# Performance work log

Hardware: AMD Instinct MI355X
Metric: run time of the kernel (lower is better)

Reference implementation:

```python
import jax, jax.numpy as jnp
import numpy as np

B, L, H = 2, 2048, 1536
I, N, R, K = 3072, 16, 96, 4


def setup_inputs() -> dict:
    key = jax.random.key(0)
    ks = jax.random.split(key, 10)
    rn = lambda k, shape, s: jax.random.normal(k, shape, jnp.float32) * s
    return {
        "hidden_states": rn(ks[0], (B, L, H), 1.0),
        "W_in": rn(ks[1], (2 * I, H), 0.02),
        "conv_w": rn(ks[2], (I, K), 0.1),
        "conv_b": rn(ks[3], (I,), 0.1),
        "W_x": rn(ks[4], (R + 2 * N, I), 0.02),
        "W_dt": rn(ks[5], (I, R), 0.02),
        "dt_bias": rn(ks[6], (I,), 0.1),
        # vLLM's weight loader stores A = -exp(A_log); replicate that here
        "A": -jnp.exp(rn(ks[7], (I, N), 0.5)),
        "D": jnp.ones((I,), jnp.float32),
        "W_out": rn(ks[8], (H, I), 0.02),
    }


def reference(hidden_states, W_in, conv_w, conv_b, W_x, W_dt, dt_bias, A, D, W_out):
    b, l, _ = hidden_states.shape
    k = conv_w.shape[1]
    n = A.shape[1]
    r = W_dt.shape[1]

    # in_proj -> [B,L,2I], split into ssm input x and gate
    proj = jnp.einsum("blh,eh->ble", hidden_states, W_in)
    x, gate = jnp.split(proj, 2, axis=-1)  # each [B,L,I]

    # causal depthwise conv1d over L (pad K-1 on the left) + SiLU
    xp = jnp.pad(x, ((0, 0), (k - 1, 0), (0, 0)))
    conv = sum(xp[:, j : j + l, :] * conv_w[:, j] for j in range(k)) + conv_b
    x = jax.nn.silu(conv)  # [B,L,I]

    # x_proj -> dt (rank R), B, C (each N)
    ssm_p = jnp.einsum("bli,pi->blp", x, W_x)
    dt_in, Bm, Cm = jnp.split(ssm_p, [r, r + n], axis=-1)

    # dt_proj (skip_bias_add) then softplus(dt + bias) inside the scan math
    dt = jnp.einsum("blr,ir->bli", dt_in, W_dt)
    delta = jax.nn.softplus(dt + dt_bias)  # [B,L,I]

    # selective scan: s_t = exp(delta_t * A) * s_{t-1} + delta_t * x_t * B_t
    def step(state, inp):
        d_t, u_t, B_t, C_t = inp  # [B,I], [B,I], [B,N], [B,N]
        dA = jnp.exp(d_t[..., None] * A)  # [B,I,N]
        state = state * dA + (d_t * u_t)[..., None] * B_t[:, None, :]
        y = jnp.einsum("bin,bn->bi", state, C_t)
        return state, y

    init = jnp.zeros((b, x.shape[-1], n), jnp.float32)
    _, ys = jax.lax.scan(
        step,
        init,
        (
            delta.transpose(1, 0, 2),
            x.transpose(1, 0, 2),
            Bm.transpose(1, 0, 2),
            Cm.transpose(1, 0, 2),
        ),
    )
    y = ys.transpose(1, 0, 2) + x * D  # skip connection via D
    y = y * jax.nn.silu(gate)

    # out_proj -> [B,L,H]
    return jnp.einsum("bli,hi->blh", y, W_out)
```

## Files before the change

kernel.cpp:

```cpp
#include <hip/hip_runtime.h>

typedef __attribute__((ext_vector_type(8))) short bf16x8;
typedef __attribute__((ext_vector_type(4))) float f32x4;

#define CCH 32
#define TCH 64

__device__ __forceinline__ unsigned short f2b(float f) {
    unsigned u = __float_as_uint(f);
    return (unsigned short)((u + 0x7fffu + ((u >> 16) & 1u)) >> 16);
}
__device__ __forceinline__ float b2f(unsigned short h) {
    return __uint_as_float(((unsigned)h) << 16);
}
__device__ __forceinline__ float softplus_f(float z) {
    return (z > 15.f) ? z : __logf(1.f + __expf(z));
}
__device__ __forceinline__ float silu_f(float g) {
    return g / (1.f + __expf(-g));
}

__device__ __forceinline__ void gload16(const unsigned short* g, unsigned short* l) {
    __builtin_amdgcn_global_load_lds(
        (const __attribute__((address_space(1))) void*)g,
        (__attribute__((address_space(3))) void*)l, 16, 0, 0);
}

__global__ __launch_bounds__(256)
void cast4(const float* __restrict__ s, unsigned short* __restrict__ d, int n4) {
    int i = blockIdx.x * 256 + threadIdx.x;
    if (i >= n4) return;
    float4 v = reinterpret_cast<const float4*>(s)[i];
    ushort4 o;
    o.x = f2b(v.x); o.y = f2b(v.y); o.z = f2b(v.z); o.w = f2b(v.w);
    reinterpret_cast<ushort4*>(d)[i] = o;
}

template <int OP>
__global__ __launch_bounds__(256)
void gemm_mfma(const unsigned short* __restrict__ A, const unsigned short* __restrict__ W,
               void* __restrict__ Cout, int Kc, int lda, int ldw, int ldc,
               const float* __restrict__ bias, int silu_col0, long long czs) {
    __shared__ unsigned short As[128 * 32];
    __shared__ unsigned short Bs[128 * 32];
    const int tid = threadIdx.x;
    const int bm = blockIdx.y * 128;
    const int bn = blockIdx.x * 128;
    const int kz = blockIdx.z;
    A += (size_t)kz * Kc;
    W += (size_t)kz * Kc;
    const int lane = tid & 63;
    const int wave = tid >> 6;
    const int r_a = lane >> 2;
    const int k8 = (lane & 3) * 8;

    unsigned short* ldsA0 = As + (size_t)(wave)     * 512;
    unsigned short* ldsA1 = As + (size_t)(wave + 4) * 512;
    unsigned short* ldsB0 = Bs + (size_t)(wave)     * 512;
    unsigned short* ldsB1 = Bs + (size_t)(wave + 4) * 512;
    const unsigned short* gA0 = A + (size_t)(bm + wave * 16 + r_a) * lda + k8;
    const unsigned short* gA1 = A + (size_t)(bm + 64 + wave * 16 + r_a) * lda + k8;
    const unsigned short* gB0 = W + (size_t)(bn + wave * 16 + r_a) * ldw + k8;
    const unsigned short* gB1 = W + (size_t)(bn + 64 + wave * 16 + r_a) * ldw + k8;

    const int wm = (wave & 1) * 64;
    const int wn = (wave >> 1) * 64;
    const int lr = lane & 15;
    const int quad = lane >> 4;

    f32x4 acc[4][4];
    const f32x4 zero = {0.f, 0.f, 0.f, 0.f};
#pragma unroll
    for (int i = 0; i < 4; i++)
#pragma unroll
        for (int j = 0; j < 4; j++) acc[i][j] = zero;

    for (int k0 = 0; k0 < Kc; k0 += 32) {
        __syncthreads();
        gload16(gA0 + k0, ldsA0);
        gload16(gA1 + k0, ldsA1);
        gload16(gB0 + k0, ldsB0);
        gload16(gB1 + k0, ldsB1);
        __syncthreads();
        bf16x8 fa[4], fb[4];
#pragma unroll
        for (int mi = 0; mi < 4; mi++)
            fa[mi] = *reinterpret_cast<const bf16x8*>(As + (wm + mi * 16 + lr) * 32 + quad * 8);
#pragma unroll
        for (int ni = 0; ni < 4; ni++)
            fb[ni] = *reinterpret_cast<const bf16x8*>(Bs + (wn + ni * 16 + lr) * 32 + quad * 8);
#pragma unroll
        for (int mi = 0; mi < 4; mi++)
#pragma unroll
            for (int ni = 0; ni < 4; ni++)
                acc[mi][ni] = __builtin_amdgcn_mfma_f32_16x16x32_bf16(fa[mi], fb[ni], acc[mi][ni], 0, 0, 0);
    }

#pragma unroll
    for (int mi = 0; mi < 4; mi++)
#pragma unroll
        for (int reg = 0; reg < 4; reg++) {
            int row = bm + wm + mi * 16 + quad * 4 + reg;
#pragma unroll
            for (int ni = 0; ni < 4; ni++) {
                int col = bn + wn + ni * 16 + lr;
                float v = acc[mi][ni][reg];
                if (OP == 0) {
                    float* Cf = (float*)Cout + (size_t)kz * czs;
                    Cf[(size_t)row * ldc + col] = v;
                } else if (OP == 2) {
                    if (col >= silu_col0) v = silu_f(v);
                    ((unsigned short*)Cout)[(size_t)row * ldc + col] = f2b(v);
                } else {
                    ((unsigned short*)Cout)[(size_t)row * ldc + col] = f2b(softplus_f(v + bias[col]));
                }
            }
        }
}

__global__ __launch_bounds__(256)
void reduce_xpart(const float* __restrict__ xpart, float* __restrict__ ssmp,
                  unsigned short* __restrict__ dtin) {
    const int BL = 4096;
    int idx = blockIdx.x * 256 + threadIdx.x;
    int row = idx >> 5;
    int c4 = (idx & 31) * 4;
    float4 s = {0.f, 0.f, 0.f, 0.f};
#pragma unroll
    for (int z = 0; z < 8; z++) {
        float4 v = *reinterpret_cast<const float4*>(xpart + (size_t)z * BL * 128 + (size_t)row * 128 + c4);
        s.x += v.x; s.y += v.y; s.z += v.z; s.w += v.w;
    }
    *reinterpret_cast<float4*>(ssmp + (size_t)row * 128 + c4) = s;
    if (c4 < 96) {
        ushort4 o;
        o.x = f2b(s.x); o.y = f2b(s.y); o.z = f2b(s.z); o.w = f2b(s.w);
        *reinterpret_cast<ushort4*>(dtin + (size_t)row * 96 + c4) = o;
    }
}

__global__ __launch_bounds__(256)
void conv_silu8(const unsigned short* __restrict__ projbf, const float* __restrict__ cw,
                const float* __restrict__ cb, unsigned short* __restrict__ xc) {
    const int I = 3072, L = 2048, LD = 6144;
    int idx = blockIdx.x * 256 + threadIdx.x;
    int i8 = (idx % (I / 8)) * 8;
    int bl = idx / (I / 8);
    int l = bl & (L - 1);
    float s[8];
    {
        float4 b0 = *reinterpret_cast<const float4*>(cb + i8);
        float4 b1 = *reinterpret_cast<const float4*>(cb + i8 + 4);
        s[0]=b0.x; s[1]=b0.y; s[2]=b0.z; s[3]=b0.w; s[4]=b1.x; s[5]=b1.y; s[6]=b1.z; s[7]=b1.w;
    }
    float w[8][4];
#pragma unroll
    for (int c = 0; c < 8; c++) {
        float4 wr = *reinterpret_cast<const float4*>(cw + (i8 + c) * 4);
        w[c][0]=wr.x; w[c][1]=wr.y; w[c][2]=wr.z; w[c][3]=wr.w;
    }
#pragma unroll
    for (int j = 0; j < 4; j++) {
        if (l + j - 3 >= 0) {
            uint4 r = *reinterpret_cast<const uint4*>(projbf + (size_t)(bl + j - 3) * LD + i8);
            float xv[8];
            xv[0]=b2f((unsigned short)(r.x & 0xffff)); xv[1]=b2f((unsigned short)(r.x >> 16));
            xv[2]=b2f((unsigned short)(r.y & 0xffff)); xv[3]=b2f((unsigned short)(r.y >> 16));
            xv[4]=b2f((unsigned short)(r.z & 0xffff)); xv[5]=b2f((unsigned short)(r.z >> 16));
            xv[6]=b2f((unsigned short)(r.w & 0xffff)); xv[7]=b2f((unsigned short)(r.w >> 16));
#pragma unroll
            for (int c = 0; c < 8; c++) s[c] = fmaf(xv[c], w[c][j], s[c]);
        }
    }
    unsigned short o[8];
#pragma unroll
    for (int c = 0; c < 8; c++) o[c] = f2b(silu_f(s[c]));
    uint4 packed;
    packed.x = (unsigned)o[0] | ((unsigned)o[1] << 16);
    packed.y = (unsigned)o[2] | ((unsigned)o[3] << 16);
    packed.z = (unsigned)o[4] | ((unsigned)o[5] << 16);
    packed.w = (unsigned)o[6] | ((unsigned)o[7] << 16);
    *reinterpret_cast<uint4*>(xc + (size_t)bl * I + i8) = packed;
}

__global__ __launch_bounds__(256)
void scan_passA(const unsigned short* __restrict__ delta_bf, const unsigned short* __restrict__ xc,
                const float* __restrict__ ssmp, const float* __restrict__ Aw,
                float* __restrict__ S_local, float* __restrict__ sumDelta) {
    const int I = 3072, L = 2048;
    __shared__ float bc[TCH][32];
    int g = blockIdx.x * 256 + threadIdx.x;
    int i = g % I;
    int bcid = g / I;
    int c = bcid % CCH;
    int b = bcid / CCH;
    size_t rowbase = (size_t)b * L + (size_t)c * TCH;
    for (int e = threadIdx.x; e < TCH * 8; e += 256) {
        int t = e >> 3, q = e & 7;
        float4 v = *reinterpret_cast<const float4*>(ssmp + (rowbase + t) * 128 + 96 + q * 4);
        *reinterpret_cast<float4*>(&bc[t][q * 4]) = v;
    }
    __syncthreads();

    float Arow[16];
#pragma unroll
    for (int n = 0; n < 16; n++) Arow[n] = Aw[i * 16 + n];
    float st[16];
#pragma unroll
    for (int n = 0; n < 16; n++) st[n] = 0.f;
    float sumD = 0.f;

    size_t rowI = rowbase * I + i;
    for (int t = 0; t < TCH; t++) {
        float delta = b2f(delta_bf[rowI]);
        float du = delta * b2f(xc[rowI]);
        sumD += delta;
        float4 b0 = *reinterpret_cast<const float4*>(&bc[t][0]);
        float4 b1 = *reinterpret_cast<const float4*>(&bc[t][4]);
        float4 b2 = *reinterpret_cast<const float4*>(&bc[t][8]);
        float4 b3 = *reinterpret_cast<const float4*>(&bc[t][12]);
        const float bv[16] = {b0.x,b0.y,b0.z,b0.w, b1.x,b1.y,b1.z,b1.w,
                              b2.x,b2.y,b2.z,b2.w, b3.x,b3.y,b3.z,b3.w};
#pragma unroll
        for (int n = 0; n < 16; n++)
            st[n] = fmaf(st[n], __expf(delta * Arow[n]), du * bv[n]);
        rowI += I;
    }
    size_t obase = (size_t)bcid * 16 * I + i;
#pragma unroll
    for (int n = 0; n < 16; n++) S_local[obase + (size_t)n * I] = st[n];
    sumDelta[(size_t)bcid * I + i] = sumD;
}

__global__ __launch_bounds__(256)
void scan_passB(const float* __restrict__ S_local, const float* __restrict__ sumDelta,
                const float* __restrict__ Aw, float* __restrict__ state_in) {
    const int I = 3072;
    int g = blockIdx.x * 256 + threadIdx.x;
    int i = g % I;
    int bn = g / I;
    int n = bn & 15;
    int b = bn >> 4;
    float a = Aw[i * 16 + n];
    float state = 0.f;
    for (int c = 0; c < CCH; c++) {
        int bcid = b * CCH + c;
        size_t idx = ((size_t)bcid * 16 + n) * I + i;
        state_in[idx] = state;
        state = fmaf(state, __expf(a * sumDelta[(size_t)bcid * I + i]), S_local[idx]);
    }
}

__global__ __launch_bounds__(256)
void scan_passC(const unsigned short* __restrict__ projbf,
                const unsigned short* __restrict__ xc,
                const float* __restrict__ ssmp, const unsigned short* __restrict__ delta_bf,
                const float* __restrict__ Aw, const float* __restrict__ Dw,
                const float* __restrict__ state_in, unsigned short* __restrict__ ybf) {
    const int I = 3072, L = 2048, LD = 6144;
    __shared__ float bc[TCH][32];
    int g = blockIdx.x * 256 + threadIdx.x;
    int i = g % I;
    int bcid = g / I;
    int c = bcid % CCH;
    int b = bcid / CCH;
    size_t rowbase = (size_t)b * L + (size_t)c * TCH;
    for (int e = threadIdx.x; e < TCH * 8; e += 256) {
        int t = e >> 3, q = e & 7;
        float4 v = *reinterpret_cast<const float4*>(ssmp + (rowbase + t) * 128 + 96 + q * 4);
        *reinterpret_cast<float4*>(&bc[t][q * 4]) = v;
    }
    __syncthreads();

    float Arow[16];
#pragma unroll
    for (int n = 0; n < 16; n++) Arow[n] = Aw[i * 16 + n];
    float Dv = Dw[i];
    float st[16];
    size_t sbase = (size_t)bcid * 16 * I + i;
#pragma unroll
    for (int n = 0; n < 16; n++) st[n] = state_in[sbase + (size_t)n * I];

    size_t rowI = rowbase * I + i;
    size_t rowG = rowbase * LD + I + i;
    for (int t = 0; t < TCH; t++) {
        float delta = b2f(delta_bf[rowI]);
        float u = b2f(xc[rowI]);
        float du = delta * u;
        float4 b0 = *reinterpret_cast<const float4*>(&bc[t][0]);
        float4 b1 = *reinterpret_cast<const float4*>(&bc[t][4]);
        float4 b2 = *reinterpret_cast<const float4*>(&bc[t][8]);
        float4 b3 = *reinterpret_cast<const float4*>(&bc[t][12]);
        float4 c0 = *reinterpret_cast<const float4*>(&bc[t][16]);
        float4 c1 = *reinterpret_cast<const float4*>(&bc[t][20]);
        float4 c2 = *reinterpret_cast<const float4*>(&bc[t][24]);
        float4 c3 = *reinterpret_cast<const float4*>(&bc[t][28]);
        const float bv[16] = {b0.x,b0.y,b0.z,b0.w, b1.x,b1.y,b1.z,b1.w,
                              b2.x,b2.y,b2.z,b2.w, b3.x,b3.y,b3.z,b3.w};
        const float cv[16] = {c0.x,c0.y,c0.z,c0.w, c1.x,c1.y,c1.z,c1.w,
                              c2.x,c2.y,c2.z,c2.w, c3.x,c3.y,c3.z,c3.w};
        float y = 0.f;
#pragma unroll
        for (int n = 0; n < 16; n++) {
            st[n] = fmaf(st[n], __expf(delta * Arow[n]), du * bv[n]);
            y = fmaf(st[n], cv[n], y);
        }
        y = fmaf(u, Dv, y);
        y *= b2f(projbf[rowG]);
        ybf[rowI] = f2b(y);
        rowI += I;
        rowG += LD;
    }
}

extern "C" void kernel_launch(void* const* d_in, const int* in_sizes, int n_in,
                              void* d_out, int out_size, void* d_ws, size_t ws_size,
                              hipStream_t stream) {
    const float* hidden  = (const float*)d_in[0];
    const float* W_in    = (const float*)d_in[1];
    const float* conv_w  = (const float*)d_in[2];
    const float* conv_b  = (const float*)d_in[3];
    const float* W_x     = (const float*)d_in[4];
    const float* W_dt    = (const float*)d_in[5];
    const float* dt_bias = (const float*)d_in[6];
    const float* Aw      = (const float*)d_in[7];
    const float* Dw      = (const float*)d_in[8];
    const float* W_out   = (const float*)d_in[9];
    float* out = (float*)d_out;

    constexpr int Bsz = 2, L = 2048, H = 1536, I = 3072, R = 96;
    constexpr int BL = Bsz * L;
    constexpr int TwoI = 2 * I;

    char* base = (char*)d_ws;
    unsigned short* proj_bf  = (unsigned short*)base; base += (size_t)BL * TwoI * 2;
    unsigned short* delta_bf = (unsigned short*)base; base += (size_t)BL * I * 2;
    unsigned short* xc_bf    = (unsigned short*)base; base += (size_t)BL * I * 2;
    unsigned short* y_bf     = (unsigned short*)base; base += (size_t)BL * I * 2;
    float* ssmp              = (float*)base;          base += (size_t)BL * 128 * 4;
    float* xpart             = (float*)base;          base += (size_t)8 * BL * 128 * 4;
    unsigned short* dtin_bf  = (unsigned short*)base; base += (size_t)BL * R * 2;
    unsigned short* wx_bf    = (unsigned short*)base; base += (size_t)128 * I * 2;
    unsigned short* wdt_bf   = (unsigned short*)base; base += (size_t)I * R * 2;
    unsigned short* wout_bf  = (unsigned short*)base; base += (size_t)H * I * 2;
    unsigned short* h_bf     = (unsigned short*)base; base += (size_t)BL * H * 2;
    unsigned short* win_bf   = (unsigned short*)base; base += (size_t)TwoI * H * 2;
    float* S_local  = (float*)h_bf;
    float* sumDelta = S_local + (size_t)Bsz * CCH * 16 * I;
    float* state_in = sumDelta + (size_t)Bsz * CCH * I;

    dim3 blk(256);

    cast4<<<(BL * H / 4 + 255) / 256, blk, 0, stream>>>(hidden, h_bf, BL * H / 4);
    cast4<<<(TwoI * H / 4 + 255) / 256, blk, 0, stream>>>(W_in, win_bf, TwoI * H / 4);
    cast4<<<(128 * I / 4 + 255) / 256, blk, 0, stream>>>(W_x, wx_bf, 128 * I / 4);
    cast4<<<(I * R / 4 + 255) / 256, blk, 0, stream>>>(W_dt, wdt_bf, I * R / 4);
    cast4<<<(H * I / 4 + 255) / 256, blk, 0, stream>>>(W_out, wout_bf, H * I / 4);

    gemm_mfma<2><<<dim3(TwoI / 128, BL / 128, 1), blk, 0, stream>>>(
        h_bf, win_bf, proj_bf, H, H, H, TwoI, nullptr, I, 0);

    conv_silu8<<<BL * I / 8 / 256, blk, 0, stream>>>(proj_bf, conv_w, conv_b, xc_bf);

    gemm_mfma<0><<<dim3(1, BL / 128, 8), blk, 0, stream>>>(
        xc_bf, wx_bf, xpart, I / 8, I, I, 128, nullptr, 0, (long long)BL * 128);
    reduce_xpart<<<BL * 32 / 256, blk, 0, stream>>>(xpart, ssmp, dtin_bf);

    gemm_mfma<3><<<dim3(I / 128, BL / 128, 1), blk, 0, stream>>>(
        dtin_bf, wdt_bf, delta_bf, R, R, R, I, dt_bias, 0, 0);

    scan_passA<<<Bsz * I * CCH / 256, blk, 0, stream>>>(
        delta_bf, xc_bf, ssmp, Aw, S_local, sumDelta);
    scan_passB<<<Bsz * 16 * I / 256, blk, 0, stream>>>(
        S_local, sumDelta, Aw, state_in);
    scan_passC<<<Bsz * I * CCH / 256, blk, 0, stream>>>(
        proj_bf, xc_bf, ssmp, delta_bf, Aw, Dw, state_in, y_bf);

    gemm_mfma<0><<<dim3(H / 128, BL / 128, 1), blk, 0, stream>>>(
        y_bf, wout_bf, out, I, I, I, H, nullptr, 0, 0);
}
```

Measured before the change: 521.1 us.

## Double-buffer GEMM LDS tiles, fuse casts, split-K out_proj with atomics

The GEMM main loop now double-buffers its LDS tiles, prefetching the next K-slice with global_load_lds while MFMAs run on the current one, which removes one barrier per iteration. The five separate fp32-to-bf16 cast launches are merged into a single kernel with hardcoded segment bounds. The output projection is split into two K halves that accumulate into a zeroed output with float atomicAdd, doubling the block count. In exchange, LDS use doubles per block, the output needs a memset, atomics add nondeterministic summation order, and the cast bounds only hold for these exact shapes.

```diff
diff --git a/kernel.cpp b/kernel.cpp
--- a/kernel.cpp
+++ b/kernel.cpp
@@ -27,13 +27,26 @@
 }
 
 __global__ __launch_bounds__(256)
-void cast4(const float* __restrict__ s, unsigned short* __restrict__ d, int n4) {
+void cast_all(const float* __restrict__ h, const float* __restrict__ win,
+              const float* __restrict__ wx, const float* __restrict__ wdt,
+              const float* __restrict__ wout,
+              unsigned short* __restrict__ dh, unsigned short* __restrict__ dwin,
+              unsigned short* __restrict__ dwx, unsigned short* __restrict__ dwdt,
+              unsigned short* __restrict__ dwout) {
+    const int n0 = 1572864, n1 = n0 + 2359296, n2 = n1 + 98304,
+              n3 = n2 + 73728, n4 = n3 + 1179648;
     int i = blockIdx.x * 256 + threadIdx.x;
-    if (i >= n4) return;
-    float4 v = reinterpret_cast<const float4*>(s)[i];
+    const float* s; unsigned short* d; int off;
+    if (i < n0)      { s = h;    d = dh;    off = i; }
+    else if (i < n1) { s = win;  d = dwin;  off = i - n0; }
+    else if (i < n2) { s = wx;   d = dwx;   off = i - n1; }
+    else if (i < n3) { s = wdt;  d = dwdt;  off = i - n2; }
+    else if (i < n4) { s = wout; d = dwout; off = i - n3; }
+    else return;
+    float4 v = reinterpret_cast<const float4*>(s)[off];
     ushort4 o;
     o.x = f2b(v.x); o.y = f2b(v.y); o.z = f2b(v.z); o.w = f2b(v.w);
-    reinterpret_cast<ushort4*>(d)[i] = o;
+    reinterpret_cast<ushort4*>(d)[off] = o;
 }
 
 template <int OP>
@@ -41,8 +54,8 @@
 void gemm_mfma(const unsigned short* __restrict__ A, const unsigned short* __restrict__ W,
                void* __restrict__ Cout, int Kc, int lda, int ldw, int ldc,
                const float* __restrict__ bias, int silu_col0, long long czs) {
-    __shared__ unsigned short As[128 * 32];
-    __shared__ unsigned short Bs[128 * 32];
+    __shared__ unsigned short As[2][128 * 32];
+    __shared__ unsigned short Bs[2][128 * 32];
     const int tid = threadIdx.x;
     const int bm = blockIdx.y * 128;
     const int bn = blockIdx.x * 128;
@@ -54,10 +67,6 @@
     const int r_a = lane >> 2;
     const int k8 = (lane & 3) * 8;
 
-    unsigned short* ldsA0 = As + (size_t)(wave)     * 512;
-    unsigned short* ldsA1 = As + (size_t)(wave + 4) * 512;
-    unsigned short* ldsB0 = Bs + (size_t)(wave)     * 512;
-    unsigned short* ldsB1 = Bs + (size_t)(wave + 4) * 512;
     const unsigned short* gA0 = A + (size_t)(bm + wave * 16 + r_a) * lda + k8;
     const unsigned short* gA1 = A + (size_t)(bm + 64 + wave * 16 + r_a) * lda + k8;
     const unsigned short* gB0 = W + (size_t)(bn + wave * 16 + r_a) * ldw + k8;
@@ -75,20 +84,31 @@
 #pragma unroll
         for (int j = 0; j < 4; j++) acc[i][j] = zero;
 
-    for (int k0 = 0; k0 < Kc; k0 += 32) {
+    const int niter = Kc >> 5;
+    gload16(gA0, As[0] + wave * 512);
+    gload16(gA1, As[0] + (wave + 4) * 512);
+    gload16(gB0, Bs[0] + wave * 512);
+    gload16(gB1, Bs[0] + (wave + 4) * 512);
+
+    for (int k = 0; k < niter; k++) {
         __syncthreads();
-        gload16(gA0 + k0, ldsA0);
-        gload16(gA1 + k0, ldsA1);
-        gload16(gB0 + k0, ldsB0);
-        gload16(gB1 + k0, ldsB1);
-        __syncthreads();
+        if (k + 1 < niter) {
+            const int off = (k + 1) << 5;
+            const int nb = (k + 1) & 1;
+            gload16(gA0 + off, As[nb] + wave * 512);
+            gload16(gA1 + off, As[nb] + (wave + 4) * 512);
+            gload16(gB0 + off, Bs[nb] + wave * 512);
+            gload16(gB1 + off, Bs[nb] + (wave + 4) * 512);
+        }
+        const unsigned short* as = As[k & 1];
+        const unsigned short* bs = Bs[k & 1];
         bf16x8 fa[4], fb[4];
 #pragma unroll
         for (int mi = 0; mi < 4; mi++)
-            fa[mi] = *reinterpret_cast<const bf16x8*>(As + (wm + mi * 16 + lr) * 32 + quad * 8);
+            fa[mi] = *reinterpret_cast<const bf16x8*>(as + (wm + mi * 16 + lr) * 32 + quad * 8);
 #pragma unroll
         for (int ni = 0; ni < 4; ni++)
-            fb[ni] = *reinterpret_cast<const bf16x8*>(Bs + (wn + ni * 16 + lr) * 32 + quad * 8);
+            fb[ni] = *reinterpret_cast<const bf16x8*>(bs + (wn + ni * 16 + lr) * 32 + quad * 8);
 #pragma unroll
         for (int mi = 0; mi < 4; mi++)
 #pragma unroll
@@ -111,8 +131,10 @@
                 } else if (OP == 2) {
                     if (col >= silu_col0) v = silu_f(v);
                     ((unsigned short*)Cout)[(size_t)row * ldc + col] = f2b(v);
+                } else if (OP == 3) {
+                    ((unsigned short*)Cout)[(size_t)row * ldc + col] = f2b(softplus_f(v + bias[col]));
                 } else {
-                    ((unsigned short*)Cout)[(size_t)row * ldc + col] = f2b(softplus_f(v + bias[col]));
+                    atomicAdd((float*)Cout + (size_t)row * ldc + col, v);
                 }
             }
         }
@@ -351,11 +373,9 @@
 
     dim3 blk(256);
 
-    cast4<<<(BL * H / 4 + 255) / 256, blk, 0, stream>>>(hidden, h_bf, BL * H / 4);
-    cast4<<<(TwoI * H / 4 + 255) / 256, blk, 0, stream>>>(W_in, win_bf, TwoI * H / 4);
-    cast4<<<(128 * I / 4 + 255) / 256, blk, 0, stream>>>(W_x, wx_bf, 128 * I / 4);
-    cast4<<<(I * R / 4 + 255) / 256, blk, 0, stream>>>(W_dt, wdt_bf, I * R / 4);
-    cast4<<<(H * I / 4 + 255) / 256, blk, 0, stream>>>(W_out, wout_bf, H * I / 4);
+    hipMemsetAsync(out, 0, (size_t)BL * H * 4, stream);
+    cast_all<<<(5283840 + 255) / 256, blk, 0, stream>>>(
+        hidden, W_in, W_x, W_dt, W_out, h_bf, win_bf, wx_bf, wdt_bf, wout_bf);
 
     gemm_mfma<2><<<dim3(TwoI / 128, BL / 128, 1), blk, 0, stream>>>(
         h_bf, win_bf, proj_bf, H, H, H, TwoI, nullptr, I, 0);
@@ -376,6 +396,6 @@
     scan_passC<<<Bsz * I * CCH / 256, blk, 0, stream>>>(
         proj_bf, xc_bf, ssmp, delta_bf, Aw, Dw, state_in, y_bf);
 
-    gemm_mfma<0><<<dim3(H / 128, BL / 128, 1), blk, 0, stream>>>(
-        y_bf, wout_bf, out, I, I, I, H, nullptr, 0, 0);
-}
+    gemm_mfma<4><<<dim3(H / 128, BL / 128, 2), blk, 0, stream>>>(
+        y_bf, wout_bf, out, I / 2, I, I, H, nullptr, 0, 0);
+}
```

Result: faster. 496.8 us (-4.7%).
